# Optimization experiments

Hardware: AMD Instinct MI355X
Metric: run time of the kernel (lower is better)

## Reference

```python
import jax, jax.numpy as jnp
import numpy as np

N_PHY = 12
NMUL = 4
WARM_UP = 365
NEARZERO = 1e-5
LENF = 15

# parameter_bounds order: BETA, FC, K0, K1, K2, LP, PERC, UZL, TT, CFMAX, CFR, CWH
PHY_LB = jnp.array([1.0, 50.0, 0.05, 0.01, 0.001, 0.2, 0.0, 0.0, -2.5, 0.5, 0.0, 0.0], dtype=jnp.float32)
PHY_UB = jnp.array([6.0, 1000.0, 0.9, 0.5, 0.2, 1.0, 10.0, 100.0, 2.5, 10.0, 0.1, 0.2], dtype=jnp.float32)
ROUTE_A_LB, ROUTE_A_UB = 0.0, 2.9
ROUTE_B_LB, ROUTE_B_UB = 0.0, 6.5


def _hbv_scan(p, t, pet, states, phy):
    """Run HBV step recurrence over time. p/t/pet: [T,G]; states: 5-tuple of [G,M]."""
    beta, fc, k0, k1, k2, lp, perc, uzl, tt, cfmax, cfr, cwh = phy  # each [G,M]

    def step(carry, xt):
        snowpack, meltwater, sm, suz, slz = carry
        Pt, Tt, PETt = xt
        Pt, Tt, PETt = Pt[:, None], Tt[:, None], PETt[:, None]  # [G,1] bcast vs [G,M]
        is_rain = (Tt >= tt).astype(sm.dtype)
        rain = Pt * is_rain
        snow = Pt * (1.0 - is_rain)
        snowpack = snowpack + snow
        melt = jnp.minimum(jnp.maximum(cfmax * (Tt - tt), 0.0), snowpack)
        meltwater = meltwater + melt
        snowpack = snowpack - melt
        refreeze = jnp.minimum(jnp.maximum(cfr * cfmax * (tt - Tt), 0.0), meltwater)
        snowpack = snowpack + refreeze
        meltwater = meltwater - refreeze
        tosoil = jnp.maximum(meltwater - cwh * snowpack, 0.0)
        meltwater = meltwater - tosoil
        soil_wetness = jnp.clip((sm / fc) ** beta, 0.0, 1.0)
        recharge = (rain + tosoil) * soil_wetness
        sm = sm + rain + tosoil - recharge
        excess = jnp.maximum(sm - fc, 0.0)
        sm = sm - excess
        evapfactor = jnp.clip(sm / (lp * fc), 0.0, 1.0)
        etact = jnp.minimum(sm, PETt * evapfactor)
        sm = jnp.maximum(sm - etact, NEARZERO)
        suz = suz + recharge + excess
        prc = jnp.minimum(suz, perc)
        suz = suz - prc
        q0 = k0 * jnp.maximum(suz - uzl, 0.0)
        suz = suz - q0
        q1 = k1 * suz
        suz = suz - q1
        slz = slz + prc
        q2 = k2 * slz
        slz = slz - q2
        return (snowpack, meltwater, sm, suz, slz), q0 + q1 + q2

    states, qs = jax.lax.scan(step, states, (p, t, pet))
    return qs, states  # qs: [T,G,M]


def _forward(x_phy, parameters):
    T, G, _ = x_phy.shape
    p, t, pet = x_phy[..., 0], x_phy[..., 1], x_phy[..., 2]
    # unpack physical params from last param timestep, map [0,1] -> bounds
    raw = parameters[-1, :, : N_PHY * NMUL].reshape(G, N_PHY, NMUL)
    phy_all = PHY_LB[None, :, None] + raw * (PHY_UB - PHY_LB)[None, :, None]
    phy = tuple(phy_all[:, i, :] for i in range(N_PHY))  # (beta, fc, k0, k1, k2, lp, perc, uzl, tt, cfmax, cfr, cwh)
    route = parameters[-1, :, N_PHY * NMUL :]
    a = ROUTE_A_LB + route[:, 0] * (ROUTE_A_UB - ROUTE_A_LB)
    b = ROUTE_B_LB + route[:, 1] * (ROUTE_B_UB - ROUTE_B_LB)

    s0 = jnp.full((G, NMUL), 0.001, dtype=x_phy.dtype)
    states = (s0, s0, s0, s0, s0)

    # warm-up under stop_gradient (matches torch.no_grad in original)
    phy_ng = jax.tree_util.tree_map(jax.lax.stop_gradient, phy)
    q_warm, states = _hbv_scan(
        jax.lax.stop_gradient(p[:WARM_UP]),
        jax.lax.stop_gradient(t[:WARM_UP]),
        jax.lax.stop_gradient(pet[:WARM_UP]),
        states, phy_ng)
    states = jax.tree_util.tree_map(jax.lax.stop_gradient, states)
    q_warm = jax.lax.stop_gradient(q_warm)

    q_pred, _ = _hbv_scan(p[WARM_UP:], t[WARM_UP:], pet[WARM_UP:], states, phy)
    qs = jnp.concatenate([q_warm, q_pred], axis=0).mean(-1)  # [T,G]

    # gamma unit hydrograph weights, [LENF, G]
    tg = (jnp.arange(LENF, dtype=qs.dtype) + 0.5)[:, None]
    aa = jax.nn.relu(a)[None, :] + 0.1
    th = jax.nn.relu(b)[None, :] + 0.5
    w = (tg ** (aa - 1.0)) * jnp.exp(-tg / th) / (jnp.exp(jax.scipy.special.gammaln(aa)) * th ** aa)
    w = w / w.sum(0)

    # causal depthwise (per-basin) convolution along time
    conv = jax.vmap(lambda q, u: jnp.convolve(q, u)[:T])(qs.T, w.T)  # [G,T]
    streamflow = conv.T[:, :, None]  # [T,G,1]
    return streamflow[WARM_UP:]


def setup_inputs() -> dict:
    key = jax.random.key(0)
    k1, k2, k3, k4 = jax.random.split(key, 4)
    T, G = 2000, 4000
    prcp = jax.random.uniform(k1, (T, G), dtype=jnp.float32) * 10.0   # mm/day
    tmean = jax.random.normal(k2, (T, G), dtype=jnp.float32) * 8.0    # degC
    pet = jax.random.uniform(k3, (T, G), dtype=jnp.float32) * 5.0     # mm/day
    x_phy = jnp.stack([prcp, tmean, pet], axis=-1)
    parameters = jax.random.uniform(k4, (1, G, N_PHY * NMUL + 2), dtype=jnp.float32)
    return {"x_phy": x_phy, "parameters": parameters}


def reference(x_phy, parameters):
    return _forward(x_phy, parameters)
```

## Files before the change

kernel.cpp:

```cpp
#include <hip/hip_runtime.h>

#define TT    2000
#define NG    4000
#define WARM  365
#define LENF  15
#define NPHY  12
#define BLK   60
#define NBLK  34
#define SLOTW 64
#define SLOT  (BLK * SLOTW)
#define ROWF  (3 * NG)

typedef const float __attribute__((address_space(1)))* gptr_t;
typedef float __attribute__((address_space(3)))* lptr_t;
typedef __attribute__((ext_vector_type(2))) float f32x2;

__device__ __forceinline__ float quad_sum(float x) {
    int a = __builtin_amdgcn_update_dpp(0, __float_as_int(x), 0xB1, 0xF, 0xF, true);
    float s = x + __int_as_float(a);
    int b = __builtin_amdgcn_update_dpp(0, __float_as_int(s), 0x4E, 0xF, 0xF, true);
    return s + __int_as_float(b);
}

#define WG_BARRIER() asm volatile("s_waitcnt lgkmcnt(0)\n\ts_barrier" ::: "memory")

__global__ __launch_bounds__(192, 1) void hbv_chain_kernel(
    const float* __restrict__ xphy,
    const float* __restrict__ prm,
    float* __restrict__ qm)
{
    __shared__ float s_stage[3 * SLOT];
    __shared__ f32x2 s_rt [2 * (BLK / 2) * 64];
    __shared__ f32x2 s_rex[2 * (BLK / 2) * 64];

    const int lane = threadIdx.x & 63;
    const int wid  = threadIdx.x >> 6;
    const int g0   = blockIdx.x * 16;
    const int cell = lane >> 2;
    const int g    = g0 + cell;
    const int m    = lane & 3;

    const float* pg = prm + (size_t)g * (NPHY * 4 + 2);

    const float lb[NPHY] = {1.0f, 50.0f, 0.05f, 0.01f, 0.001f, 0.2f, 0.0f, 0.0f, -2.5f, 0.5f, 0.0f, 0.0f};
    const float ub[NPHY] = {6.0f, 1000.0f, 0.9f, 0.5f, 0.2f, 1.0f, 10.0f, 100.0f, 2.5f, 10.0f, 0.1f, 0.2f};
    float ph[NPHY];
    #pragma unroll
    for (int i = 0; i < NPHY; ++i)
        ph[i] = lb[i] + pg[i * 4 + m] * (ub[i] - lb[i]);

    const float beta = ph[0], fc = ph[1], k0 = ph[2], k1 = ph[3], k2 = ph[4],
                lp = ph[5], perc = ph[6], uzl = ph[7], ttp = ph[8],
                cfmax = ph[9], cfr = ph[10], cwh = ph[11];
    const float rlpfc  = 1.0f / (lp * fc);
    const float cfrcf  = cfr * cfmax;
    const float blfc   = beta * __builtin_amdgcn_logf(1.0f / fc);
    const float onemk1 = 1.0f - k1;
    const float onemk2 = 1.0f - k2;

    float snowpack = 0.001f, meltwater = 0.001f;
    float sm = 0.001f;
    float suz = 0.001f, slz = 0.001f;

    const int loffd = (lane < 48 ? lane : 47);

    auto stage_blk = [&](int b) {
        const int tb = b * BLK + wid * 20;
        float* ldst = &s_stage[(b % 3) * SLOT + (wid * 20) * SLOTW];
        #pragma unroll
        for (int c = 0; c < 20; ++c) {
            int t = tb + c; t = (t < TT) ? t : (TT - 1);
            const float* src = xphy + (size_t)t * ROWF + g0 * 3 + loffd;
            __builtin_amdgcn_global_load_lds((gptr_t)src, (lptr_t)(ldst + c * SLOTW), 4, 0, 0);
        }
    };

    stage_blk(0);
    asm volatile("s_waitcnt vmcnt(0)" ::: "memory");
    WG_BARRIER();

    for (int i = 0; i <= NBLK + 1; ++i) {
        if (i < NBLK - 1) stage_blk(i + 1);

        if (wid == 0) {
            if (i < NBLK) {
                const float* sb = &s_stage[(i % 3) * SLOT + cell * 3];
                f32x2* rtw = &s_rt[(i & 1) * ((BLK / 2) * 64) + lane];
                float rt_even = 0.0f;
                #pragma unroll
                for (int j = 0; j < BLK; ++j) {
                    const float Pt = sb[j * SLOTW];
                    const float Tm = sb[j * SLOTW + 1];
                    const float dT      = Tm - ttp;
                    const float rain    = (Tm >= ttp) ? Pt : 0.0f;
                    const float snw     = Pt - rain;
                    const float meltcap = cfmax * fmaxf(dT, 0.0f);
                    const float refcap  = cfrcf * fmaxf(-dT, 0.0f);
                    snowpack += snw;
                    const float melt = fminf(meltcap, snowpack);
                    meltwater += melt;
                    snowpack  -= melt;
                    const float refreeze = fminf(refcap, meltwater);
                    meltwater -= refreeze;
                    snowpack  += refreeze;
                    const float tosoil = fmaxf(fmaf(-cwh, snowpack, meltwater), 0.0f);
                    meltwater -= tosoil;
                    const float rt = rain + tosoil;
                    if ((j & 1) == 0) rt_even = rt;
                    else { f32x2 pr; pr[0] = rt_even; pr[1] = rt; rtw[(j >> 1) * 64] = pr; }
                }
            }
        } else if (wid == 1) {
            const int b = i - 1;
            if (b >= 0 && b < NBLK) {
                const float* sbe = &s_stage[(b % 3) * SLOT + cell * 3 + 2];
                const f32x2* rtr = &s_rt[(b & 1) * ((BLK / 2) * 64) + lane];
                f32x2* rexw = &s_rex[(b & 1) * ((BLK / 2) * 64) + lane];
                f32x2 rp; rp[0] = 0.0f; rp[1] = 0.0f;
                float rex_even = 0.0f;
                #pragma unroll
                for (int j = 0; j < BLK; ++j) {
                    if ((j & 1) == 0) rp = rtr[(j >> 1) * 64];
                    const float rt = ((j & 1) == 0) ? rp[0] : rp[1];
                    const float ev = sbe[j * SLOTW];
                    const float sw    = __builtin_amdgcn_exp2f(fmaf(beta, __builtin_amdgcn_logf(sm), blfc));
                    const float sp    = sm + rt;
                    const float sm1   = fmaf(-rt, sw, sp);
                    const float sm2   = fminf(sm1, fc);
                    const float uf    = fmaxf(fmaf(-ev, rlpfc, 1.0f), 0.0f);
                    sm = fmaxf(fmaxf(sm2 * uf, sm2 - ev), 1e-5f);
                    const float rex = fmaf(rt, sw, sm1 - sm2);
                    if ((j & 1) == 0) rex_even = rex;
                    else { f32x2 pr; pr[0] = rex_even; pr[1] = rex; rexw[(j >> 1) * 64] = pr; }
                }
            }
        } else {
            const int b = i - 2;
            if (b >= 0 && b < NBLK) {
                const int t0 = b * BLK;
                const f32x2* rexr = &s_rex[(b & 1) * ((BLK / 2) * 64) + lane];
                f32x2 rp; rp[0] = 0.0f; rp[1] = 0.0f;
                float ov[BLK / 4];
                #pragma unroll
                for (int k = 0; k < BLK / 4; ++k) ov[k] = 0.0f;
                #pragma unroll
                for (int j = 0; j < BLK; ++j) {
                    if ((j & 1) == 0) rp = rexr[(j >> 1) * 64];
                    const float rex = ((j & 1) == 0) ? rp[0] : rp[1];
                    const float suz1 = suz + rex;
                    const float prc  = fminf(suz1, perc);
                    const float suzA = suz1 - prc;
                    const float tq   = fmaxf(suzA - uzl, 0.0f);
                    const float q0   = k0 * tq;
                    const float suzB = fmaf(-k0, tq, suzA);
                    const float q1   = k1 * suzB;
                    suz = suzB * onemk1;
                    const float sl1  = slz + prc;
                    const float q2   = k2 * sl1;
                    slz = sl1 * onemk2;
                    const float q = quad_sum(q0 + q1 + q2);
                    const bool sel = ((j & 3) == m);
                    ov[j >> 2] = sel ? q : ov[j >> 2];
                }
                #pragma unroll
                for (int k = 0; k < BLK / 4; ++k) {
                    const int t = t0 + k * 4 + m;
                    if (t < TT) qm[(size_t)t * NG + g] = ov[k];
                }
            }
        }

        asm volatile("s_waitcnt vmcnt(0)" ::: "memory");
        WG_BARRIER();
    }
}

__global__ __launch_bounds__(256) void hbv_conv_kernel(
    const float* __restrict__ qm,
    const float* __restrict__ prm,
    float* __restrict__ out)
{
    const int g = blockIdx.x * 256 + threadIdx.x;
    if (g >= NG) return;
    const int t0 = WARM + blockIdx.y * 8;

    const float* pr = prm + (size_t)g * 50;
    const float aa  = fmaxf(pr[48] * 2.9f, 0.0f) + 0.1f;
    const float th  = fmaxf(pr[49] * 6.5f, 0.0f) + 0.5f;
    const float aam1 = aa - 1.0f;
    const float rthl = 1.4426950408889634f / th;

    const float L2TG[LENF] = {
        -1.0f, 0.5849625007211562f, 1.3219280948873623f, 1.8073549220576042f,
        2.169925001442312f, 2.4594316186372973f, 2.700439718141092f,
        2.9068905956085187f, 3.087462841250339f, 3.247927513443585f,
        3.3923174227787602f, 3.523561956057013f, 3.643856189774724f,
        3.754887502163468f, 3.857980995127572f };

    float w[LENF];
    float wsum = 0.0f;
    #pragma unroll
    for (int k = 0; k < LENF; ++k) {
        const float tg = (float)k + 0.5f;
        w[k] = __builtin_amdgcn_exp2f(fmaf(aam1, L2TG[k], -tg * rthl));
        wsum += w[k];
    }
    const float rw = 0.25f / wsum;

    float qv[22];
    #pragma unroll
    for (int j = 0; j < 22; ++j) {
        int t = t0 - 14 + j; t = (t < TT) ? t : (TT - 1);
        qv[j] = qm[(size_t)t * NG + g];
    }
    #pragma unroll
    for (int c = 0; c < 8; ++c) {
        float o = 0.0f;
        #pragma unroll
        for (int k = 0; k < LENF; ++k)
            o = fmaf(w[k], qv[14 + c - k], o);
        const int t = t0 + c;
        if (t < TT) out[(size_t)(t - WARM) * NG + g] = o * rw;
    }
}

extern "C" void kernel_launch(void* const* d_in, const int* in_sizes, int n_in,
                              void* d_out, int out_size, void* d_ws, size_t ws_size,
                              hipStream_t stream) {
    const float* xphy = (const float*)d_in[0];
    const float* prm  = (const float*)d_in[1];
    float* out = (float*)d_out;
    float* qm  = (float*)d_ws;

    hbv_chain_kernel<<<NG / 16, 192, 0, stream>>>(xphy, prm, qm);

    dim3 grid2((NG + 255) / 256, (TT - WARM + 7) / 8);
    hbv_conv_kernel<<<grid2, 256, 0, stream>>>(qm, prm, out);
}
```

Baseline: 142.9 us.

## Process two basins per lane in HBV chain kernel and restage input loads

Each workgroup now handles 32 basins instead of 16, so every lane runs two independent recurrence chains (A and B) interleaved. The goal is instruction-level parallelism that hides the latency of the serial snow, soil and response recurrences. The block length drops from 60 to 40 steps and the staging load is rewritten as a flat, contiguous copy split across two waves, with the output wave no longer waiting on vmcnt. In exchange the kernel uses more registers and launches half as many workgroups (125 on a large GPU), which lowers occupancy and parallel coverage.

```diff
diff --git a/kernel.cpp b/kernel.cpp
--- a/kernel.cpp
+++ b/kernel.cpp
@@ -5,10 +5,11 @@
 #define WARM  365
 #define LENF  15
 #define NPHY  12
-#define BLK   60
-#define NBLK  34
-#define SLOTW 64
-#define SLOT  (BLK * SLOTW)
+#define BLK   40
+#define NBLK  50
+#define STW   96
+#define SLOT  (BLK * STW)
+#define PAIRS (BLK / 2)
 #define ROWF  (3 * NG)
 
 typedef const float __attribute__((address_space(1)))* gptr_t;
@@ -30,147 +31,204 @@
     float* __restrict__ qm)
 {
     __shared__ float s_stage[3 * SLOT];
-    __shared__ f32x2 s_rt [2 * (BLK / 2) * 64];
-    __shared__ f32x2 s_rex[2 * (BLK / 2) * 64];
-
-    const int lane = threadIdx.x & 63;
-    const int wid  = threadIdx.x >> 6;
-    const int g0   = blockIdx.x * 16;
-    const int cell = lane >> 2;
-    const int g    = g0 + cell;
-    const int m    = lane & 3;
-
-    const float* pg = prm + (size_t)g * (NPHY * 4 + 2);
+    __shared__ f32x2 s_rt [2 * PAIRS * 128];
+    __shared__ f32x2 s_rex[2 * PAIRS * 128];
+
+    const int lane  = threadIdx.x & 63;
+    const int wid   = threadIdx.x >> 6;
+    const int g0    = blockIdx.x * 32;
+    const int cellA = lane >> 2;
+    const int cellB = cellA + 16;
+    const int m     = lane & 3;
+    const int gA    = g0 + cellA;
+    const int gB    = g0 + cellB;
+
+    const float* pgA = prm + (size_t)gA * 50;
+    const float* pgB = prm + (size_t)gB * 50;
 
     const float lb[NPHY] = {1.0f, 50.0f, 0.05f, 0.01f, 0.001f, 0.2f, 0.0f, 0.0f, -2.5f, 0.5f, 0.0f, 0.0f};
     const float ub[NPHY] = {6.0f, 1000.0f, 0.9f, 0.5f, 0.2f, 1.0f, 10.0f, 100.0f, 2.5f, 10.0f, 0.1f, 0.2f};
-    float ph[NPHY];
-    #pragma unroll
-    for (int i = 0; i < NPHY; ++i)
-        ph[i] = lb[i] + pg[i * 4 + m] * (ub[i] - lb[i]);
-
-    const float beta = ph[0], fc = ph[1], k0 = ph[2], k1 = ph[3], k2 = ph[4],
-                lp = ph[5], perc = ph[6], uzl = ph[7], ttp = ph[8],
-                cfmax = ph[9], cfr = ph[10], cwh = ph[11];
-    const float rlpfc  = 1.0f / (lp * fc);
-    const float cfrcf  = cfr * cfmax;
-    const float blfc   = beta * __builtin_amdgcn_logf(1.0f / fc);
-    const float onemk1 = 1.0f - k1;
-    const float onemk2 = 1.0f - k2;
-
-    float snowpack = 0.001f, meltwater = 0.001f;
-    float sm = 0.001f;
-    float suz = 0.001f, slz = 0.001f;
-
-    const int loffd = (lane < 48 ? lane : 47);
+    float phA[NPHY], phB[NPHY];
+    #pragma unroll
+    for (int i = 0; i < NPHY; ++i) {
+        phA[i] = lb[i] + pgA[i * 4 + m] * (ub[i] - lb[i]);
+        phB[i] = lb[i] + pgB[i * 4 + m] * (ub[i] - lb[i]);
+    }
+    const float betaA = phA[0], fcA = phA[1], k0A = phA[2], k1A = phA[3], k2A = phA[4],
+                lpA = phA[5], percA = phA[6], uzlA = phA[7], ttpA = phA[8],
+                cfmaxA = phA[9], cwhA = phA[11];
+    const float betaB = phB[0], fcB = phB[1], k0B = phB[2], k1B = phB[3], k2B = phB[4],
+                lpB = phB[5], percB = phB[6], uzlB = phB[7], ttpB = phB[8],
+                cfmaxB = phB[9], cwhB = phB[11];
+    const float cfrcfA = phA[10] * cfmaxA, cfrcfB = phB[10] * cfmaxB;
+    const float rlpfcA = 1.0f / (lpA * fcA), rlpfcB = 1.0f / (lpB * fcB);
+    const float blfcA  = betaA * __builtin_amdgcn_logf(1.0f / fcA);
+    const float blfcB  = betaB * __builtin_amdgcn_logf(1.0f / fcB);
+    const float onemk1A = 1.0f - k1A, onemk1B = 1.0f - k1B;
+    const float onemk2A = 1.0f - k2A, onemk2B = 1.0f - k2B;
+
+    float spA = 0.001f, mwA = 0.001f, spB = 0.001f, mwB = 0.001f;
+    float smA = 0.001f, smB = 0.001f;
+    float suzA = 0.001f, slzA = 0.001f, suzB = 0.001f, slzB = 0.001f;
+
+    int doff[30];
+    #pragma unroll
+    for (int ld = 0; ld < 30; ++ld) {
+        const int flat = (wid * 30 + ld) * 64 + lane;
+        const int st   = flat / 96;
+        doff[ld] = st * ROWF + (flat - st * 96);
+    }
 
     auto stage_blk = [&](int b) {
-        const int tb = b * BLK + wid * 20;
-        float* ldst = &s_stage[(b % 3) * SLOT + (wid * 20) * SLOTW];
+        const float* xblk = xphy + (size_t)b * (BLK * ROWF) + g0 * 3;
+        float* lb0 = &s_stage[(b % 3) * SLOT];
         #pragma unroll
-        for (int c = 0; c < 20; ++c) {
-            int t = tb + c; t = (t < TT) ? t : (TT - 1);
-            const float* src = xphy + (size_t)t * ROWF + g0 * 3 + loffd;
-            __builtin_amdgcn_global_load_lds((gptr_t)src, (lptr_t)(ldst + c * SLOTW), 4, 0, 0);
+        for (int ld = 0; ld < 30; ++ld) {
+            __builtin_amdgcn_global_load_lds((gptr_t)(xblk + doff[ld]),
+                (lptr_t)(lb0 + (wid * 30 + ld) * 64), 4, 0, 0);
         }
     };
 
-    stage_blk(0);
-    asm volatile("s_waitcnt vmcnt(0)" ::: "memory");
+#define SNOWSTEP(P_, T_, ttp_, cfmax_, cfrcf_, cwh_, sp_, mw_, RT_) do {    \
+    const float dT_   = (T_) - (ttp_);                                      \
+    const float rain_ = ((T_) >= (ttp_)) ? (P_) : 0.0f;                     \
+    const float snw_  = (P_) - rain_;                                       \
+    const float mc_   = (cfmax_) * fmaxf(dT_, 0.0f);                        \
+    const float rc_   = (cfrcf_) * fmaxf(-dT_, 0.0f);                       \
+    (sp_) += snw_;                                                          \
+    const float melt_ = fminf(mc_, (sp_));                                  \
+    (mw_) += melt_;                                                         \
+    (sp_) -= melt_;                                                         \
+    const float rf_ = fminf(rc_, (mw_));                                    \
+    (mw_) -= rf_;                                                           \
+    (sp_) += rf_;                                                           \
+    const float ts_ = fmaxf(fmaf(-(cwh_), (sp_), (mw_)), 0.0f);             \
+    (mw_) -= ts_;                                                           \
+    (RT_) = rain_ + ts_;                                                    \
+} while (0)
+
+#define SOILSTEP(RT_, EV_, beta_, blfc_, fc_, rlpfc_, sm_, REX_) do {       \
+    const float sw_  = __builtin_amdgcn_exp2f(fmaf((beta_),                 \
+                         __builtin_amdgcn_logf((sm_)), (blfc_)));           \
+    const float sp_  = (sm_) + (RT_);                                       \
+    const float sm1_ = fmaf(-(RT_), sw_, sp_);                              \
+    const float sm2_ = fminf(sm1_, (fc_));                                  \
+    const float uf_  = fmaxf(fmaf(-(EV_), (rlpfc_), 1.0f), 0.0f);           \
+    (sm_) = fmaxf(fmaxf(sm2_ * uf_, sm2_ - (EV_)), 1e-5f);                  \
+    (REX_) = fmaf((RT_), sw_, sm1_ - sm2_);                                 \
+} while (0)
+
+#define RESPSTEP(REX_, perc_, uzl_, k0_, k1_, k2_, o1_, o2_, suz_, slz_, Q_) do { \
+    const float s1_ = (suz_) + (REX_);                                      \
+    const float pc_ = fminf(s1_, (perc_));                                  \
+    const float sA_ = s1_ - pc_;                                            \
+    const float tq_ = fmaxf(sA_ - (uzl_), 0.0f);                            \
+    const float q0_ = (k0_) * tq_;                                          \
+    const float sB_ = fmaf(-(k0_), tq_, sA_);                               \
+    const float q1_ = (k1_) * sB_;                                          \
+    (suz_) = sB_ * (o1_);                                                   \
+    const float sl_ = (slz_) + pc_;                                         \
+    const float q2_ = (k2_) * sl_;                                          \
+    (slz_) = sl_ * (o2_);                                                   \
+    (Q_) = q0_ + q1_ + q2_;                                                 \
+} while (0)
+
+    if (wid < 2) {
+        stage_blk(0);
+        asm volatile("s_waitcnt vmcnt(0)" ::: "memory");
+    }
     WG_BARRIER();
 
     for (int i = 0; i <= NBLK + 1; ++i) {
-        if (i < NBLK - 1) stage_blk(i + 1);
-
         if (wid == 0) {
+            if (i + 1 < NBLK) stage_blk(i + 1);
             if (i < NBLK) {
-                const float* sb = &s_stage[(i % 3) * SLOT + cell * 3];
-                f32x2* rtw = &s_rt[(i & 1) * ((BLK / 2) * 64) + lane];
-                float rt_even = 0.0f;
+                const float* sb = &s_stage[(i % 3) * SLOT];
+                f32x2* rtw = &s_rt[(i & 1) * (PAIRS * 128)];
+                float reA = 0.0f, reB = 0.0f;
                 #pragma unroll
                 for (int j = 0; j < BLK; ++j) {
-                    const float Pt = sb[j * SLOTW];
-                    const float Tm = sb[j * SLOTW + 1];
-                    const float dT      = Tm - ttp;
-                    const float rain    = (Tm >= ttp) ? Pt : 0.0f;
-                    const float snw     = Pt - rain;
-                    const float meltcap = cfmax * fmaxf(dT, 0.0f);
-                    const float refcap  = cfrcf * fmaxf(-dT, 0.0f);
-                    snowpack += snw;
-                    const float melt = fminf(meltcap, snowpack);
-                    meltwater += melt;
-                    snowpack  -= melt;
-                    const float refreeze = fminf(refcap, meltwater);
-                    meltwater -= refreeze;
-                    snowpack  += refreeze;
-                    const float tosoil = fmaxf(fmaf(-cwh, snowpack, meltwater), 0.0f);
-                    meltwater -= tosoil;
-                    const float rt = rain + tosoil;
-                    if ((j & 1) == 0) rt_even = rt;
-                    else { f32x2 pr; pr[0] = rt_even; pr[1] = rt; rtw[(j >> 1) * 64] = pr; }
+                    const float PA = sb[j * STW + cellA * 3];
+                    const float TA = sb[j * STW + cellA * 3 + 1];
+                    const float PB = sb[j * STW + cellB * 3];
+                    const float TB = sb[j * STW + cellB * 3 + 1];
+                    float rtA, rtB;
+                    SNOWSTEP(PA, TA, ttpA, cfmaxA, cfrcfA, cwhA, spA, mwA, rtA);
+                    SNOWSTEP(PB, TB, ttpB, cfmaxB, cfrcfB, cwhB, spB, mwB, rtB);
+                    if ((j & 1) == 0) { reA = rtA; reB = rtB; }
+                    else {
+                        f32x2 a; a[0] = reA; a[1] = rtA; rtw[(j >> 1) * 128 + lane] = a;
+                        f32x2 b; b[0] = reB; b[1] = rtB; rtw[(j >> 1) * 128 + 64 + lane] = b;
+                    }
                 }
             }
+            asm volatile("s_waitcnt vmcnt(0)" ::: "memory");
         } else if (wid == 1) {
+            if (i + 1 < NBLK) stage_blk(i + 1);
             const int b = i - 1;
             if (b >= 0 && b < NBLK) {
-                const float* sbe = &s_stage[(b % 3) * SLOT + cell * 3 + 2];
-                const f32x2* rtr = &s_rt[(b & 1) * ((BLK / 2) * 64) + lane];
-                f32x2* rexw = &s_rex[(b & 1) * ((BLK / 2) * 64) + lane];
-                f32x2 rp; rp[0] = 0.0f; rp[1] = 0.0f;
-                float rex_even = 0.0f;
+                const float* sbe = &s_stage[(b % 3) * SLOT];
+                const f32x2* rtr = &s_rt[(b & 1) * (PAIRS * 128)];
+                f32x2* rexw = &s_rex[(b & 1) * (PAIRS * 128)];
+                f32x2 rpA, rpB;
+                rpA[0] = 0.0f; rpA[1] = 0.0f; rpB = rpA;
+                float xeA = 0.0f, xeB = 0.0f;
                 #pragma unroll
                 for (int j = 0; j < BLK; ++j) {
-                    if ((j & 1) == 0) rp = rtr[(j >> 1) * 64];
-                    const float rt = ((j & 1) == 0) ? rp[0] : rp[1];
-                    const float ev = sbe[j * SLOTW];
-                    const float sw    = __builtin_amdgcn_exp2f(fmaf(beta, __builtin_amdgcn_logf(sm), blfc));
-                    const float sp    = sm + rt;
-                    const float sm1   = fmaf(-rt, sw, sp);
-                    const float sm2   = fminf(sm1, fc);
-                    const float uf    = fmaxf(fmaf(-ev, rlpfc, 1.0f), 0.0f);
-                    sm = fmaxf(fmaxf(sm2 * uf, sm2 - ev), 1e-5f);
-                    const float rex = fmaf(rt, sw, sm1 - sm2);
-                    if ((j & 1) == 0) rex_even = rex;
-                    else { f32x2 pr; pr[0] = rex_even; pr[1] = rex; rexw[(j >> 1) * 64] = pr; }
+                    if ((j & 1) == 0) {
+                        rpA = rtr[(j >> 1) * 128 + lane];
+                        rpB = rtr[(j >> 1) * 128 + 64 + lane];
+                    }
+                    const float rtA = ((j & 1) == 0) ? rpA[0] : rpA[1];
+                    const float rtB = ((j & 1) == 0) ? rpB[0] : rpB[1];
+                    const float evA = sbe[j * STW + cellA * 3 + 2];
+                    const float evB = sbe[j * STW + cellB * 3 + 2];
+                    float rxA, rxB;
+                    SOILSTEP(rtA, evA, betaA, blfcA, fcA, rlpfcA, smA, rxA);
+                    SOILSTEP(rtB, evB, betaB, blfcB, fcB, rlpfcB, smB, rxB);
+                    if ((j & 1) == 0) { xeA = rxA; xeB = rxB; }
+                    else {
+                        f32x2 a; a[0] = xeA; a[1] = rxA; rexw[(j >> 1) * 128 + lane] = a;
+                        f32x2 b2; b2[0] = xeB; b2[1] = rxB; rexw[(j >> 1) * 128 + 64 + lane] = b2;
+                    }
                 }
             }
+            asm volatile("s_waitcnt vmcnt(0)" ::: "memory");
         } else {
             const int b = i - 2;
             if (b >= 0 && b < NBLK) {
                 const int t0 = b * BLK;
-                const f32x2* rexr = &s_rex[(b & 1) * ((BLK / 2) * 64) + lane];
-                f32x2 rp; rp[0] = 0.0f; rp[1] = 0.0f;
-                float ov[BLK / 4];
-                #pragma unroll
-                for (int k = 0; k < BLK / 4; ++k) ov[k] = 0.0f;
+                const f32x2* rexr = &s_rex[(b & 1) * (PAIRS * 128)];
+                f32x2 rpA, rpB;
+                rpA[0] = 0.0f; rpA[1] = 0.0f; rpB = rpA;
+                float ovA[BLK / 4], ovB[BLK / 4];
+                #pragma unroll
+                for (int k = 0; k < BLK / 4; ++k) { ovA[k] = 0.0f; ovB[k] = 0.0f; }
                 #pragma unroll
                 for (int j = 0; j < BLK; ++j) {
-                    if ((j & 1) == 0) rp = rexr[(j >> 1) * 64];
-                    const float rex = ((j & 1) == 0) ? rp[0] : rp[1];
-                    const float suz1 = suz + rex;
-                    const float prc  = fminf(suz1, perc);
-                    const float suzA = suz1 - prc;
-                    const float tq   = fmaxf(suzA - uzl, 0.0f);
-                    const float q0   = k0 * tq;
-                    const float suzB = fmaf(-k0, tq, suzA);
-                    const float q1   = k1 * suzB;
-                    suz = suzB * onemk1;
-                    const float sl1  = slz + prc;
-                    const float q2   = k2 * sl1;
-                    slz = sl1 * onemk2;
-                    const float q = quad_sum(q0 + q1 + q2);
+                    if ((j & 1) == 0) {
+                        rpA = rexr[(j >> 1) * 128 + lane];
+                        rpB = rexr[(j >> 1) * 128 + 64 + lane];
+                    }
+                    const float rxA = ((j & 1) == 0) ? rpA[0] : rpA[1];
+                    const float rxB = ((j & 1) == 0) ? rpB[0] : rpB[1];
+                    float qA, qB;
+                    RESPSTEP(rxA, percA, uzlA, k0A, k1A, k2A, onemk1A, onemk2A, suzA, slzA, qA);
+                    RESPSTEP(rxB, percB, uzlB, k0B, k1B, k2B, onemk1B, onemk2B, suzB, slzB, qB);
+                    qA = quad_sum(qA);
+                    qB = quad_sum(qB);
                     const bool sel = ((j & 3) == m);
-                    ov[j >> 2] = sel ? q : ov[j >> 2];
+                    ovA[j >> 2] = sel ? qA : ovA[j >> 2];
+                    ovB[j >> 2] = sel ? qB : ovB[j >> 2];
                 }
                 #pragma unroll
                 for (int k = 0; k < BLK / 4; ++k) {
                     const int t = t0 + k * 4 + m;
-                    if (t < TT) qm[(size_t)t * NG + g] = ov[k];
+                    qm[(size_t)t * NG + gA] = ovA[k];
+                    qm[(size_t)t * NG + gB] = ovB[k];
                 }
             }
         }
-
-        asm volatile("s_waitcnt vmcnt(0)" ::: "memory");
         WG_BARRIER();
     }
 }
@@ -232,7 +290,7 @@
     float* out = (float*)d_out;
     float* qm  = (float*)d_ws;
 
-    hbv_chain_kernel<<<NG / 16, 192, 0, stream>>>(xphy, prm, qm);
+    hbv_chain_kernel<<<NG / 32, 192, 0, stream>>>(xphy, prm, qm);
 
     dim3 grid2((NG + 255) / 256, (TT - WARM + 7) / 8);
     hbv_conv_kernel<<<grid2, 256, 0, stream>>>(qm, prm, out);
```

After: 221.7 us. 55.1% more time.
